# Optimization experiments

Hardware: AMD Instinct MI355X
Metric: run time of the kernel (lower is better)

The kernel has to match this reference:

```python
import jax, jax.numpy as jnp
import numpy as np

EPS = 1e-6
NUM_SEMANTICS = 8
HIDDEN = 768
BATCH = 4096


def _gram_schmidt_single(vectors, fallback):
    """Sequential (classical, per-torch-code) Gram-Schmidt on (S, D) vectors.
    fallback: (S, D) random vectors used when a residual norm falls below EPS.
    """
    S = vectors.shape[0]
    qs = []
    for i in range(S):
        v = vectors[i]
        for j in range(i):
            qj = qs[j]
            denom = jnp.dot(qj, qj)
            safe_denom = jnp.where(denom > 0, denom, 1.0)
            proj = jnp.dot(v, qj) / safe_denom
            # torch: only subtract if ||q_j|| > eps
            v = jnp.where(jnp.sqrt(denom) > EPS, v - proj * qj, v)
        norm = jnp.linalg.norm(v)
        safe_norm = jnp.where(norm > 0, norm, 1.0)
        fb = fallback[i]
        fb = fb / jnp.linalg.norm(fb)
        q = jnp.where(norm > EPS, v / safe_norm, fb)
        qs.append(q)
    return jnp.stack(qs, axis=0)


def setup_inputs() -> dict:
    key = jax.random.key(0)
    semantic_reprs = jax.random.normal(key, (BATCH, NUM_SEMANTICS, HIDDEN), dtype=jnp.float32)
    return {"semantic_reprs": semantic_reprs}


def reference(semantic_reprs):
    B, S, D = semantic_reprs.shape
    # fixed fallback random vectors (stand-in for torch.randn_like in the degenerate branch)
    fallback = jax.random.normal(jax.random.key(42), (B, S, D), dtype=semantic_reprs.dtype)
    return jax.vmap(_gram_schmidt_single)(semantic_reprs, fallback)
```

## Files before the change

### kernel.cpp

```cpp
#include <hip/hip_runtime.h>


#define S_VECS 8
#define D_DIM 768
#define CHUNKS 192

typedef float f32x4 __attribute__((ext_vector_type(4)));

__device__ __forceinline__ float wave_reduce_sum(float x) {
#pragma unroll
    for (int off = 32; off >= 1; off >>= 1)
        x += __shfl_xor(x, off, 64);
    return x;
}

__device__ __forceinline__ void process_store(float (&v)[S_VECS][4],
                                              float (*red)[S_VECS][3],
                                              int wave, int lane, int w1, int w2,
                                              float* __restrict__ out,
                                              size_t b, int chunk) {
    float inv_n[S_VECS];

#pragma unroll
    for (int i = 1; i < S_VECS; ++i) {
        const int p = i & 1;
        float d[S_VECS];
#pragma unroll
        for (int j = 0; j < S_VECS; ++j) {
            if (j < i) {
                float acc = 0.f;
#pragma unroll
                for (int e = 0; e < 4; ++e) acc += v[i][e] * v[j][e];
                d[j] = acc;
            }
        }
        float self = 0.f;
#pragma unroll
        for (int e = 0; e < 4; ++e) self += v[i - 1][e] * v[i - 1][e];

#pragma unroll
        for (int j = 0; j < S_VECS; ++j) {
            if (j < i) d[j] = wave_reduce_sum(d[j]);
        }
        self = wave_reduce_sum(self);

        if (lane == 0) {
#pragma unroll
            for (int j = 0; j < S_VECS; ++j) {
                if (j < i) red[p][j][wave] = d[j];
            }
            red[p][i][wave] = self;
        }
        __syncthreads();
#pragma unroll
        for (int j = 0; j < S_VECS; ++j) {
            if (j < i) d[j] += red[p][j][w1] + red[p][j][w2];
        }
        self += red[p][i][w1] + red[p][i][w2];
        inv_n[i - 1] = 1.0f / self;

#pragma unroll
        for (int j = 0; j < S_VECS; ++j) {
            if (j < i) {
                const float proj = d[j] * inv_n[j];
#pragma unroll
                for (int e = 0; e < 4; ++e) v[i][e] -= proj * v[j][e];
            }
        }
    }
    {
        float self = 0.f;
#pragma unroll
        for (int e = 0; e < 4; ++e) self += v[S_VECS - 1][e] * v[S_VECS - 1][e];
        self = wave_reduce_sum(self);
        if (lane == 0) red[0][0][wave] = self;
        __syncthreads();
        self += red[0][0][w1] + red[0][0][w2];
        inv_n[S_VECS - 1] = 1.0f / self;
    }

    f32x4* dst = reinterpret_cast<f32x4*>(out) + b * (S_VECS * CHUNKS);
#pragma unroll
    for (int s = 0; s < S_VECS; ++s) {
        const float inv_norm = sqrtf(inv_n[s]);
        f32x4 f;
        f.x = v[s][0] * inv_norm;
        f.y = v[s][1] * inv_norm;
        f.z = v[s][2] * inv_norm;
        f.w = v[s][3] * inv_norm;
        dst[s * CHUNKS + chunk] = f;
    }
}

__global__ __launch_bounds__(192)
void gram_schmidt_kernel(const float* __restrict__ in, float* __restrict__ out) {
    const int wave = threadIdx.x >> 6;
    const int lane = threadIdx.x & 63;
    const int chunk = wave * 64 + lane;

    __shared__ float red[2][S_VECS][3];
    const int w1 = (wave == 2) ? 0 : wave + 1;
    const int w2 = (wave == 0) ? 2 : wave - 1;

    const size_t bA = (size_t)blockIdx.x * 2;
    const size_t bB = bA + 1;

    float vA[S_VECS][4], vB[S_VECS][4];
    const f32x4* srcA = reinterpret_cast<const f32x4*>(in) + bA * (S_VECS * CHUNKS);
    const f32x4* srcB = reinterpret_cast<const f32x4*>(in) + bB * (S_VECS * CHUNKS);
#pragma unroll
    for (int s = 0; s < S_VECS; ++s) {
        f32x4 f = srcA[s * CHUNKS + chunk];
        vA[s][0] = f.x; vA[s][1] = f.y; vA[s][2] = f.z; vA[s][3] = f.w;
    }
#pragma unroll
    for (int s = 0; s < S_VECS; ++s) {
        f32x4 f = srcB[s * CHUNKS + chunk];
        vB[s][0] = f.x; vB[s][1] = f.y; vB[s][2] = f.z; vB[s][3] = f.w;
    }

    process_store(vA, red, wave, lane, w1, w2, out, bA, chunk);
    process_store(vB, red, wave, lane, w1, w2, out, bB, chunk);
}

extern "C" void kernel_launch(void* const* d_in, const int* in_sizes, int n_in,
                              void* d_out, int out_size, void* d_ws, size_t ws_size,
                              hipStream_t stream) {
    const float* in = (const float*)d_in[0];
    float* out = (float*)d_out;
    const int B = in_sizes[0] / (S_VECS * D_DIM);
    gram_schmidt_kernel<<<B / 2, 192, 0, stream>>>(in, out);
}
```

Baseline: 49.55 us.

## Interleave two batch items' Gram-Schmidt to share barriers and add nontemporal stores

Processes both batch elements assigned to a block in lockstep instead of sequentially, so each of the eight cross-wave reductions handles both items under one __syncthreads, halving barrier count and interleaving independent shuffle chains for ILP. Loads of both items are interleaved, and output writes use nontemporal stores to avoid cache pollution. The cost is higher register pressure from keeping two sets of dot products live at once.

```diff
diff --git a/kernel.cpp b/kernel.cpp
--- a/kernel.cpp
+++ b/kernel.cpp
@@ -2,7 +2,6 @@
 
 
 #define S_VECS 8
-#define D_DIM 768
 #define CHUNKS 192
 
 typedef float f32x4 __attribute__((ext_vector_type(4)));
@@ -14,91 +13,13 @@
     return x;
 }
 
-__device__ __forceinline__ void process_store(float (&v)[S_VECS][4],
-                                              float (*red)[S_VECS][3],
-                                              int wave, int lane, int w1, int w2,
-                                              float* __restrict__ out,
-                                              size_t b, int chunk) {
-    float inv_n[S_VECS];
-
-#pragma unroll
-    for (int i = 1; i < S_VECS; ++i) {
-        const int p = i & 1;
-        float d[S_VECS];
-#pragma unroll
-        for (int j = 0; j < S_VECS; ++j) {
-            if (j < i) {
-                float acc = 0.f;
-#pragma unroll
-                for (int e = 0; e < 4; ++e) acc += v[i][e] * v[j][e];
-                d[j] = acc;
-            }
-        }
-        float self = 0.f;
-#pragma unroll
-        for (int e = 0; e < 4; ++e) self += v[i - 1][e] * v[i - 1][e];
-
-#pragma unroll
-        for (int j = 0; j < S_VECS; ++j) {
-            if (j < i) d[j] = wave_reduce_sum(d[j]);
-        }
-        self = wave_reduce_sum(self);
-
-        if (lane == 0) {
-#pragma unroll
-            for (int j = 0; j < S_VECS; ++j) {
-                if (j < i) red[p][j][wave] = d[j];
-            }
-            red[p][i][wave] = self;
-        }
-        __syncthreads();
-#pragma unroll
-        for (int j = 0; j < S_VECS; ++j) {
-            if (j < i) d[j] += red[p][j][w1] + red[p][j][w2];
-        }
-        self += red[p][i][w1] + red[p][i][w2];
-        inv_n[i - 1] = 1.0f / self;
-
-#pragma unroll
-        for (int j = 0; j < S_VECS; ++j) {
-            if (j < i) {
-                const float proj = d[j] * inv_n[j];
-#pragma unroll
-                for (int e = 0; e < 4; ++e) v[i][e] -= proj * v[j][e];
-            }
-        }
-    }
-    {
-        float self = 0.f;
-#pragma unroll
-        for (int e = 0; e < 4; ++e) self += v[S_VECS - 1][e] * v[S_VECS - 1][e];
-        self = wave_reduce_sum(self);
-        if (lane == 0) red[0][0][wave] = self;
-        __syncthreads();
-        self += red[0][0][w1] + red[0][0][w2];
-        inv_n[S_VECS - 1] = 1.0f / self;
-    }
-
-    f32x4* dst = reinterpret_cast<f32x4*>(out) + b * (S_VECS * CHUNKS);
-#pragma unroll
-    for (int s = 0; s < S_VECS; ++s) {
-        const float inv_norm = sqrtf(inv_n[s]);
-        f32x4 f;
-        f.x = v[s][0] * inv_norm;
-        f.y = v[s][1] * inv_norm;
-        f.z = v[s][2] * inv_norm;
-        f.w = v[s][3] * inv_norm;
-        dst[s * CHUNKS + chunk] = f;
-    }
-}
-
 __global__ __launch_bounds__(192)
 void gram_schmidt_kernel(const float* __restrict__ in, float* __restrict__ out) {
     const int wave = threadIdx.x >> 6;
     const int lane = threadIdx.x & 63;
     const int chunk = wave * 64 + lane;
 
-    __shared__ float red[2][S_VECS][3];
+    __shared__ float red[2][2][S_VECS][3];
     const int w1 = (wave == 2) ? 0 : wave + 1;
     const int w2 = (wave == 0) ? 2 : wave - 1;
 
@@ -110,17 +31,111 @@
     const f32x4* srcB = reinterpret_cast<const f32x4*>(in) + bB * (S_VECS * CHUNKS);
 #pragma unroll
     for (int s = 0; s < S_VECS; ++s) {
-        f32x4 f = srcA[s * CHUNKS + chunk];
-        vA[s][0] = f.x; vA[s][1] = f.y; vA[s][2] = f.z; vA[s][3] = f.w;
+        f32x4 fa = srcA[s * CHUNKS + chunk];
+        f32x4 fb = srcB[s * CHUNKS + chunk];
+        vA[s][0] = fa.x; vA[s][1] = fa.y; vA[s][2] = fa.z; vA[s][3] = fa.w;
+        vB[s][0] = fb.x; vB[s][1] = fb.y; vB[s][2] = fb.z; vB[s][3] = fb.w;
     }
+
+    float inv_nA[S_VECS], inv_nB[S_VECS];
+
+#pragma unroll
+    for (int i = 1; i < S_VECS; ++i) {
+        const int p = i & 1;
+
+        float dA[S_VECS], dB[S_VECS];
+#pragma unroll
+        for (int j = 0; j < S_VECS; ++j) {
+            if (j < i) {
+                float a = 0.f, b2 = 0.f;
+#pragma unroll
+                for (int e = 0; e < 4; ++e) {
+                    a += vA[i][e] * vA[j][e];
+                    b2 += vB[i][e] * vB[j][e];
+                }
+                dA[j] = a; dB[j] = b2;
+            }
+        }
+        float selfA = 0.f, selfB = 0.f;
+#pragma unroll
+        for (int e = 0; e < 4; ++e) {
+            selfA += vA[i - 1][e] * vA[i - 1][e];
+            selfB += vB[i - 1][e] * vB[i - 1][e];
+        }
+
+#pragma unroll
+        for (int j = 0; j < S_VECS; ++j) {
+            if (j < i) { dA[j] = wave_reduce_sum(dA[j]); dB[j] = wave_reduce_sum(dB[j]); }
+        }
+        selfA = wave_reduce_sum(selfA);
+        selfB = wave_reduce_sum(selfB);
+
+        if (lane == 0) {
+#pragma unroll
+            for (int j = 0; j < S_VECS; ++j) {
+                if (j < i) { red[p][0][j][wave] = dA[j]; red[p][1][j][wave] = dB[j]; }
+            }
+            red[p][0][i][wave] = selfA;
+            red[p][1][i][wave] = selfB;
+        }
+        __syncthreads();
+#pragma unroll
+        for (int j = 0; j < S_VECS; ++j) {
+            if (j < i) {
+                dA[j] += red[p][0][j][w1] + red[p][0][j][w2];
+                dB[j] += red[p][1][j][w1] + red[p][1][j][w2];
+            }
+        }
+        selfA += red[p][0][i][w1] + red[p][0][i][w2];
+        selfB += red[p][1][i][w1] + red[p][1][i][w2];
+        inv_nA[i - 1] = 1.0f / selfA;
+        inv_nB[i - 1] = 1.0f / selfB;
+
+#pragma unroll
+        for (int j = 0; j < S_VECS; ++j) {
+            if (j < i) {
+                const float pA = dA[j] * inv_nA[j];
+                const float pB = dB[j] * inv_nB[j];
+#pragma unroll
+                for (int e = 0; e < 4; ++e) {
+                    vA[i][e] -= pA * vA[j][e];
+                    vB[i][e] -= pB * vB[j][e];
+                }
+            }
+        }
+    }
+
+    {
+        float selfA = 0.f, selfB = 0.f;
+#pragma unroll
+        for (int e = 0; e < 4; ++e) {
+            selfA += vA[S_VECS - 1][e] * vA[S_VECS - 1][e];
+            selfB += vB[S_VECS - 1][e] * vB[S_VECS - 1][e];
+        }
+        selfA = wave_reduce_sum(selfA);
+        selfB = wave_reduce_sum(selfB);
+        if (lane == 0) { red[0][0][0][wave] = selfA; red[0][1][0][wave] = selfB; }
+        __syncthreads();
+        selfA += red[0][0][0][w1] + red[0][0][0][w2];
+        selfB += red[0][1][0][w1] + red[0][1][0][w2];
+        inv_nA[S_VECS - 1] = 1.0f / selfA;
+        inv_nB[S_VECS - 1] = 1.0f / selfB;
+    }
+
+    f32x4* dstA = reinterpret_cast<f32x4*>(out) + bA * (S_VECS * CHUNKS);
+    f32x4* dstB = reinterpret_cast<f32x4*>(out) + bB * (S_VECS * CHUNKS);
 #pragma unroll
     for (int s = 0; s < S_VECS; ++s) {
-        f32x4 f = srcB[s * CHUNKS + chunk];
-        vB[s][0] = f.x; vB[s][1] = f.y; vB[s][2] = f.z; vB[s][3] = f.w;
+        const float inA = sqrtf(inv_nA[s]);
+        const float inB = sqrtf(inv_nB[s]);
+        f32x4 fa, fb;
+        fa.x = vA[s][0] * inA; fa.y = vA[s][1] * inA;
+        fa.z = vA[s][2] * inA; fa.w = vA[s][3] * inA;
+        fb.x = vB[s][0] * inB; fb.y = vB[s][1] * inB;
+        fb.z = vB[s][2] * inB; fb.w = vB[s][3] * inB;
+        __builtin_nontemporal_store(fa, &dstA[s * CHUNKS + chunk]);
+        __builtin_nontemporal_store(fb, &dstB[s * CHUNKS + chunk]);
     }
-
-    process_store(vA, red, wave, lane, w1, w2, out, bA, chunk);
-    process_store(vB, red, wave, lane, w1, w2, out, bB, chunk);
 }
 
 extern "C" void kernel_launch(void* const* d_in, const int* in_sizes, int n_in,
@@ -128,6 +143,6 @@
                               hipStream_t stream) {
     const float* in = (const float*)d_in[0];
     float* out = (float*)d_out;
-    const int B = in_sizes[0] / (S_VECS * D_DIM);
+    const int B = in_sizes[0] / (S_VECS * 768);
     gram_schmidt_kernel<<<B / 2, 192, 0, stream>>>(in, out);
 }
```

New measurement: 45.85 us. 1.08x faster.
